# Kernel optimization log

Measured on AMD Instinct MI355X. Metric: run time of the kernel, lower is better.

The kernel has to match this reference:

```python
import jax, jax.numpy as jnp
import numpy as np

N_QUBITS = 14
N_LAYERS = 4
BATCH = 2048
DIM = 2 ** N_QUBITS


def setup_inputs() -> dict:
    key = jax.random.key(0)
    k1, k2 = jax.random.split(key)
    x = jax.random.normal(k1, (BATCH, N_QUBITS), dtype=jnp.float32)
    params = 2.0 * jnp.pi * jax.random.uniform(k2, (N_LAYERS, 1, N_QUBITS), dtype=jnp.float32)
    return {"x": x, "params": params}


def _angle_embed_x(x):
    """RX(x_q) angle embedding from |0...0>: product state, qubit 0 most significant."""
    B, n = x.shape
    c = jnp.cos(x / 2)
    s = jnp.sin(x / 2)
    state = jnp.ones((B, 1), dtype=jnp.complex64)
    for q in range(n):  # fixed small loop over qubits (kron build-up)
        amp = jnp.stack([c[:, q] + 0j, (-1j) * s[:, q]], axis=-1).astype(jnp.complex64)  # (B,2)
        state = (state[:, :, None] * amp[:, None, :]).reshape(B, -1)
    return state  # (B, 2^n)


def _apply_rx(state, theta, q, n):
    """Apply RX(theta) on qubit q to batched state (B, 2^n)."""
    c = jnp.cos(theta / 2).astype(jnp.complex64)
    s = ((-1j) * jnp.sin(theta / 2)).astype(jnp.complex64)
    B = state.shape[0]
    st = state.reshape(B, 2 ** q, 2, 2 ** (n - q - 1))
    a0, a1 = st[:, :, 0, :], st[:, :, 1, :]
    new = jnp.stack([c * a0 + s * a1, s * a0 + c * a1], axis=2)
    return new.reshape(B, -1)


def _apply_cnot(state, ctrl, tgt, n):
    B = state.shape[0]
    lo, hi = min(ctrl, tgt), max(ctrl, tgt)
    st = state.reshape(B, 2 ** lo, 2, 2 ** (hi - lo - 1), 2, 2 ** (n - hi - 1))
    if ctrl < tgt:
        # control axis=2, target axis=4: flip target where control==1
        flipped = st[:, :, 1, :, ::-1, :]
        st = jnp.stack([st[:, :, 0], flipped], axis=2)
    else:
        # control axis=4, target axis=2
        flipped = st[:, :, ::-1, :, 1, :]
        st = jnp.stack([st[:, :, :, :, 0, :], flipped], axis=4)
    return st.reshape(B, -1)


def _z_signs(n):
    # sign[q, k] = +1 if bit q (MSB-first) of k is 0 else -1
    k = np.arange(2 ** n)
    bits = (k[None, :] >> np.arange(n - 1, -1, -1)[:, None]) & 1
    return jnp.asarray(1.0 - 2.0 * bits, dtype=jnp.float32)  # (n, 2^n)


def reference(x, params):
    n = N_QUBITS
    state = _angle_embed_x(x)  # (B, 2^n) complex64
    for layer in range(N_LAYERS):
        w = params[layer, 0]  # (n,)
        for q in range(n):
            state = _apply_rx(state, w[q], q, n)
        for q in range(n):  # ring of CNOTs (basic entangling layer)
            state = _apply_cnot(state, q, (q + 1) % n, n)
    probs = state.real ** 2 + state.imag ** 2  # (B, 2^n)
    return probs @ _z_signs(n).T  # (B, n) per-qubit <Z>
```

## Files before the change

### kernel.cpp

```cpp
#include <hip/hip_runtime.h>
#include <hip/hip_fp16.h>
#include <stdint.h>

#define NQ     14
#define NL     4
#define BATCH  2048
#define DIM    16384

using half8  = __attribute__((ext_vector_type(8)))  _Float16;
using half4  = __attribute__((ext_vector_type(4)))  _Float16;
using f32x16 = __attribute__((ext_vector_type(16))) float;
using f32x4  = __attribute__((ext_vector_type(4)))  float;

constexpr uint32_t mmask(int b) { return b < 13 ? (((1u << (b + 1)) - 1u) | 0x2000u) : 0x1FFFu; }
constexpr uint32_t laddr(uint32_t a) {
  uint32_t col = a >> 5;
  uint32_t g = (a >> 2) & 7u;
  const uint32_t mx[9] = {1u, 2u, 4u, 2u, 0u, 0u, 1u, 2u, 4u};
  for (int j = 0; j < 9; ++j) if ((col >> j) & 1u) g ^= mx[j];
  return (col << 7) ^ (g << 4) ^ ((a & 3u) << 2);
}
constexpr uint32_t IMG(int b) { return laddr(mmask(b)); }

struct TabEmb { uint32_t v[32]; constexpr TabEmb() : v() {
  for (int k = 0; k < 32; ++k) { uint32_t x = 0;
    for (int b = 0; b < 5; ++b) if ((k >> b) & 1) x ^= IMG(b); v[k] = x; } } };
constexpr TabEmb EMBT{};

struct TabSc { uint32_t v[8][4]; constexpr TabSc() : v() {
  for (int i = 0; i < 8; ++i) for (int r = 0; r < 4; ++r) { uint32_t x = 0;
    if (r & 1) x ^= IMG(0); if (r & 2) x ^= IMG(1);
    if (i & 1) x ^= IMG(4); if (i & 2) x ^= IMG(5); if (i & 4) x ^= IMG(6);
    v[i][r] = x; } } };
constexpr TabSc SCT{};

struct TabEc { uint32_t v[16]; constexpr TabEc() : v() {
  for (int e = 0; e < 16; ++e) { uint32_t ce = (uint32_t)((e & 3) | ((e >> 2) << 3));
    v[e] = (ce << 6) ^ (((ce ^ (ce >> 2)) & 3u) << 4); } } };
constexpr TabEc ECT{};

__device__ __forceinline__ half8 h8(uint32_t a, uint32_t b, uint32_t c, uint32_t d) {
  union { uint32_t u[4]; half8 h; } z; z.u[0]=a; z.u[1]=b; z.u[2]=c; z.u[3]=d; return z.h; }
__device__ __forceinline__ half4 h4v(uint32_t a, uint32_t b) {
  union { uint32_t u[2]; half4 h; } z; z.u[0]=a; z.u[1]=b; return z.h; }
__device__ __forceinline__ uint4 ld16(const char* p) {
  return *(const uint4*)__builtin_assume_aligned(p, 16); }
__device__ __forceinline__ void st16(char* p, uint4 v) {
  *(uint4*)__builtin_assume_aligned(p, 16) = v; }
__device__ __forceinline__ uint32_t pkh2(float a, float b) {
  return __builtin_bit_cast(uint32_t, __floats2half2_rn(a, b)); }

__global__ void uprep_kernel(const float* __restrict__ params, __half* __restrict__ U) {
  const int id = blockIdx.x * 256 + threadIdx.x;
  int li, grp, r, k, nb, off, mstride;
  if (id < 6144) { li = id >> 11; const int sub = id & 2047;
    grp = sub >> 10; const int cell = sub & 1023; r = cell >> 5; k = cell & 31; nb = 5;
    off = li * 4608 + grp * 2048 + r * 32 + k; mstride = 1024; }
  else { const int id2 = id - 6144; li = id2 >> 8; const int cell = id2 & 255;
    grp = 2; r = cell >> 4; k = cell & 15; nb = 4;
    off = li * 4608 + 4096 + r * 16 + k; mstride = 256; }
  const float* th = params + (li + 1) * NQ;
  float mag = 1.f; int d = 0;
  for (int j = 0; j < nb; ++j) {
    const int pbit = (grp == 0) ? j : (grp == 1) ? 5 + j : 10 + j;
    const float ph = 0.5f * th[13 - pbit];
    const int df = ((r >> j) ^ (k >> j)) & 1;
    mag *= df ? sinf(ph) : cosf(ph);
    d += df;
  }
  float R = 0.f, I = 0.f;
  switch (d & 3) { case 0: R = mag; break; case 1: I = -mag; break;
                   case 2: R = -mag; break; default: I = mag; break; }
  U[off] = __float2half_rn(R);
  U[off + mstride] = __float2half_rn(I);
}

__global__ __launch_bounds__(512)
__attribute__((amdgpu_waves_per_eu(4, 4)))
void qsim_kernel(const float* __restrict__ x, const float* __restrict__ params,
                 const __half* __restrict__ U, float* __restrict__ out) {
  __shared__ uint32_t lds[DIM];
  __shared__ float red[8][16];
  __shared__ float exc[NQ], exs[NQ];
  char* const sb = (char*)lds;

  const int b = blockIdx.x;
  const int t = threadIdx.x;
  const int w = t >> 6, l = t & 63;
  const int hi = l >> 5, l31 = l & 31, l15 = l & 15, h4 = (l >> 4) & 3;
  const int swz = (l & 7) ^ ((l >> 2) & 2) ^ w;

  if (t < NQ) { const float xv = x[b * NQ + t] + params[t];
                exc[t] = cosf(0.5f * xv); exs[t] = sinf(0.5f * xv); }
  __syncthreads();

  const uint32_t colAB = (uint32_t)(((w << 6) | l31) << 7);
  const uint32_t sgl = (uint32_t)(((l15 ^ (l15 >> 2)) ^ w) & 3);
  const uint32_t gcr = (uint32_t)((w << 13) | (l15 << 6) | (((h4 ^ (int)sgl) & 3) << 4));
  const uint32_t lbc = ((uint32_t)l31 << 11) ^ ((uint32_t)hi << 8)
      ^ ((uint32_t)(((w >> 1) ^ ((l31 >> 2) & 3) ^ hi) & 3) << 4)
      ^ ((uint32_t)(((w << 1) ^ l) & 3) << 2);
  uint32_t scb = 0;
  { if (l & 16) scb ^= IMG(2);
    if (l & 32) scb ^= IMG(3);
#pragma unroll
    for (int j = 0; j < 4; ++j) if ((l15 >> j) & 1) scb ^= IMG(10 + j);
#pragma unroll
    for (int j = 0; j < 3; ++j) if ((w >> j) & 1) scb ^= IMG(7 + j); }

  const bool gcs0 = (l & 1), gcs1 = (l & 2);
  const uint32_t scb2 = scb ^ (gcs0 ? IMG(0) : 0u) ^ (gcs1 ? IMG(1) : 0u);
  const bool gbs0 = (l & 16), gbs1 = (l & 4);
  const uint32_t lbc2 = lbc ^ (gbs0 ? 0x50u : 0u) ^ (gbs1 ? 0xA0u : 0u);

  {
    float pb = 1.f;
#pragma unroll
    for (int j = 0; j < 9; ++j) pb *= ((t >> j) & 1) ? exs[8 - j] : exc[8 - j];
    uint32_t eb = 0;
#pragma unroll
    for (int j = 0; j < 9; ++j) if ((t >> j) & 1) eb ^= IMG(5 + j);
    const int tt = t & 31;
    const int sgk = ((tt & 1) ? 16 : 0) | ((tt & 2) ? 4 : 0) | ((tt & 4) ? 8 : 0)
                  | ((tt & 8) ? 2 : 0) | ((tt & 16) ? 1 : 0);
    if (sgk & 1)  eb ^= IMG(0);
    if (sgk & 2)  eb ^= IMG(1);
    if (sgk & 4)  eb ^= IMG(2);
    if (sgk & 8)  eb ^= IMG(3);
    if (sgk & 16) eb ^= IMG(4);
    const int pct = __popc(t);
#pragma unroll
    for (int k = 0; k < 32; ++k) {
      const int idx = k ^ sgk;
      float f = pb;
      f *= (idx & 1)  ? exs[13] : exc[13];
      f *= (idx & 2)  ? exs[12] : exc[12];
      f *= (idx & 4)  ? exs[11] : exc[11];
      f *= (idx & 8)  ? exs[10] : exc[10];
      f *= (idx & 16) ? exs[9]  : exc[9];
      const int pc = (pct + __popc(idx)) & 3;
      const float xr = (pc == 0) ? f : ((pc == 2) ? -f : 0.f);
      const float yi = (pc == 1) ? -f : ((pc == 3) ? f : 0.f);
      *(uint32_t*)(sb + (eb ^ EMBT.v[k])) = pkh2(xr, yi);
    }
  }
  __syncthreads();

#pragma unroll 1
  for (int li = 0; li < 3; ++li) {
    const __half* Ul = U + li * 4608;

    {
      half8 bR[2], bI[2];
#pragma unroll
      for (int s = 0; s < 2; ++s) {
        const __half* up = Ul + l31 * 32 + s * 16 + hi * 8;
        bR[s] = *(const half8*)__builtin_assume_aligned(up, 16);
        bI[s] = *(const half8*)__builtin_assume_aligned(up + 1024, 16);
      }
#pragma unroll
      for (int n = 0; n < 2; ++n) {
        const uint32_t cb = colAB + (uint32_t)(n << 12);
        f32x16 cX = {}, cY = {};
#pragma unroll
        for (int s = 0; s < 2; ++s) {
          const uint4 q0 = ld16(sb + cb + (uint32_t)((((s << 2) + (hi << 1) + 0) ^ swz) << 4));
          const uint4 q1 = ld16(sb + cb + (uint32_t)((((s << 2) + (hi << 1) + 1) ^ swz) << 4));
          const uint32_t dw[8] = {q0.x, q0.y, q0.z, q0.w, q1.x, q1.y, q1.z, q1.w};
          uint32_t ax[4], ay[4], an[4];
#pragma unroll
          for (int j = 0; j < 4; ++j) {
            ax[j] = __builtin_amdgcn_perm(dw[2 * j + 1], dw[2 * j], 0x05040100u);
            ay[j] = __builtin_amdgcn_perm(dw[2 * j + 1], dw[2 * j], 0x07060302u);
            an[j] = ay[j] ^ 0x80008000u;
          }
          const half8 aX = h8(ax[0], ax[1], ax[2], ax[3]);
          const half8 aY = h8(ay[0], ay[1], ay[2], ay[3]);
          const half8 aN = h8(an[0], an[1], an[2], an[3]);
          cX = __builtin_amdgcn_mfma_f32_32x32x16_f16(aX, bR[s], cX, 0, 0, 0);
          cX = __builtin_amdgcn_mfma_f32_32x32x16_f16(aN, bI[s], cX, 0, 0, 0);
          cY = __builtin_amdgcn_mfma_f32_32x32x16_f16(aX, bI[s], cY, 0, 0, 0);
          cY = __builtin_amdgcn_mfma_f32_32x32x16_f16(aY, bR[s], cY, 0, 0, 0);
        }
#pragma unroll
        for (int u = 0; u < 4; ++u) {
          uint4 o;
          o.x = pkh2(cX[4 * u + 0], cY[4 * u + 0]); o.y = pkh2(cX[4 * u + 1], cY[4 * u + 1]);
          o.z = pkh2(cX[4 * u + 2], cY[4 * u + 2]); o.w = pkh2(cX[4 * u + 3], cY[4 * u + 3]);
          st16(sb + cb + (uint32_t)((((u << 1) + hi) ^ swz) << 4), o);
        }
      }
      __builtin_amdgcn_wave_barrier();
    }

    {
      half8 bR[2], bI[2];
#pragma unroll
      for (int s = 0; s < 2; ++s) {
        const __half* up = Ul + 2048 + l31 * 32 + s * 16 + hi * 8;
        bR[s] = *(const half8*)__builtin_assume_aligned(up, 16);
        bI[s] = *(const half8*)__builtin_assume_aligned(up + 1024, 16);
      }
      uint4 dr[2][2][2];
#pragma unroll
      for (int n = 0; n < 2; ++n)
#pragma unroll
        for (int s = 0; s < 2; ++s)
#pragma unroll
          for (int j = 0; j < 2; ++j)
            dr[n][s][j] = ld16(sb + colAB + (uint32_t)(n << 12)
                               + (uint32_t)((((s << 2) + (hi << 1) + j) ^ swz) << 4));
      __syncthreads();
#pragma unroll
      for (int n = 0; n < 2; ++n) {
        f32x16 cX = {}, cY = {};
#pragma unroll
        for (int s = 0; s < 2; ++s) {
          const uint32_t dw[8] = {dr[n][s][0].x, dr[n][s][0].y, dr[n][s][0].z, dr[n][s][0].w,
                                  dr[n][s][1].x, dr[n][s][1].y, dr[n][s][1].z, dr[n][s][1].w};
          uint32_t ax[4], ay[4], an[4];
#pragma unroll
          for (int j = 0; j < 4; ++j) {
            ax[j] = __builtin_amdgcn_perm(dw[2 * j + 1], dw[2 * j], 0x05040100u);
            ay[j] = __builtin_amdgcn_perm(dw[2 * j + 1], dw[2 * j], 0x07060302u);
            an[j] = ay[j] ^ 0x80008000u;
          }
          const half8 aX = h8(ax[0], ax[1], ax[2], ax[3]);
          const half8 aY = h8(ay[0], ay[1], ay[2], ay[3]);
          const half8 aN = h8(an[0], an[1], an[2], an[3]);
          cX = __builtin_amdgcn_mfma_f32_32x32x16_f16(aX, bR[s], cX, 0, 0, 0);
          cX = __builtin_amdgcn_mfma_f32_32x32x16_f16(aN, bI[s], cX, 0, 0, 0);
          cY = __builtin_amdgcn_mfma_f32_32x32x16_f16(aX, bI[s], cY, 0, 0, 0);
          cY = __builtin_amdgcn_mfma_f32_32x32x16_f16(aY, bR[s], cY, 0, 0, 0);
        }
        const uint32_t lb = lbc2 ^ (uint32_t)(n << 2);
        uint32_t pk[16];
#pragma unroll
        for (int e = 0; e < 16; ++e) pk[e] = pkh2(cX[e], cY[e]);
#pragma unroll
        for (int q = 0; q < 4; ++q) {
          const uint32_t a0 = pk[4 * q + 0], a1 = pk[4 * q + 1];
          const uint32_t a2 = pk[4 * q + 2], a3 = pk[4 * q + 3];
          const uint32_t b0 = gbs0 ? a1 : a0, b1 = gbs0 ? a0 : a1;
          const uint32_t b2 = gbs0 ? a3 : a2, b3 = gbs0 ? a2 : a3;
          const uint32_t c0 = gbs1 ? b2 : b0, c1 = gbs1 ? b3 : b1;
          const uint32_t c2 = gbs1 ? b0 : b2, c3 = gbs1 ? b1 : b3;
          *(uint32_t*)(sb + (lb ^ ECT.v[4 * q + 0])) = c0;
          *(uint32_t*)(sb + (lb ^ ECT.v[4 * q + 1])) = c1;
          *(uint32_t*)(sb + (lb ^ ECT.v[4 * q + 2])) = c2;
          *(uint32_t*)(sb + (lb ^ ECT.v[4 * q + 3])) = c3;
        }
      }
      __syncthreads();
    }

    {
      const __half* up = Ul + 4096 + l15 * 16 + h4 * 4;
      const half4 bR = *(const half4*)__builtin_assume_aligned(up, 8);
      const half4 bI = *(const half4*)__builtin_assume_aligned(up + 256, 8);
      uint4 dc[8];
#pragma unroll
      for (int i = 0; i < 8; ++i)
        dc[i] = ld16(sb + gcr + (uint32_t)(i << 10));
      __syncthreads();
      float sE0[8], sE1[8], sE2[8];
#pragma unroll
      for (int i = 0; i < 8; ++i) {
        const int m2 = (i >> 1) & 3;
        const uint32_t ph[4] = {dc[i].x, dc[i].y, dc[i].z, dc[i].w};
        const uint32_t d0 = ph[0 ^ m2], d1 = ph[1 ^ m2], d2 = ph[2 ^ m2], d3 = ph[3 ^ m2];
        const uint32_t x0 = __builtin_amdgcn_perm(d1, d0, 0x05040100u);
        const uint32_t x1 = __builtin_amdgcn_perm(d3, d2, 0x05040100u);
        const uint32_t y0 = __builtin_amdgcn_perm(d1, d0, 0x07060302u);
        const uint32_t y1 = __builtin_amdgcn_perm(d3, d2, 0x07060302u);
        const half4 aX = h4v(x0, x1);
        const half4 aY = h4v(y0, y1);
        const half4 aN = h4v(y0 ^ 0x80008000u, y1 ^ 0x80008000u);
        f32x4 cX = {}, cY = {};
        cX = __builtin_amdgcn_mfma_f32_16x16x16f16(aX, bR, cX, 0, 0, 0);
        cX = __builtin_amdgcn_mfma_f32_16x16x16f16(aN, bI, cX, 0, 0, 0);
        cY = __builtin_amdgcn_mfma_f32_16x16x16f16(aX, bI, cY, 0, 0, 0);
        cY = __builtin_amdgcn_mfma_f32_16x16x16f16(aY, bR, cY, 0, 0, 0);
        if (li < 2) {
          const uint32_t p0 = pkh2(cX[0], cY[0]), p1 = pkh2(cX[1], cY[1]);
          const uint32_t p2 = pkh2(cX[2], cY[2]), p3 = pkh2(cX[3], cY[3]);
          const uint32_t q0 = gcs0 ? p1 : p0, q1 = gcs0 ? p0 : p1;
          const uint32_t q2 = gcs0 ? p3 : p2, q3 = gcs0 ? p2 : p3;
          const uint32_t r0 = gcs1 ? q2 : q0, r1 = gcs1 ? q3 : q1;
          const uint32_t r2 = gcs1 ? q0 : q2, r3 = gcs1 ? q1 : q3;
          *(uint32_t*)(sb + (scb2 ^ SCT.v[i][0])) = r0;
          *(uint32_t*)(sb + (scb2 ^ SCT.v[i][1])) = r1;
          *(uint32_t*)(sb + (scb2 ^ SCT.v[i][2])) = r2;
          *(uint32_t*)(sb + (scb2 ^ SCT.v[i][3])) = r3;
        } else {
          const float p0 = fmaf(cX[0], cX[0], cY[0] * cY[0]);
          const float p1 = fmaf(cX[1], cX[1], cY[1] * cY[1]);
          const float p2 = fmaf(cX[2], cX[2], cY[2] * cY[2]);
          const float p3 = fmaf(cX[3], cX[3], cY[3] * cY[3]);
          const float t01 = p0 + p1, t23 = p2 + p3;
          const float d01 = p0 - p1, d23 = p2 - p3;
          sE0[i] = t01 + t23;
          sE1[i] = t01 - t23;
          sE2[i] = d01 - d23;
        }
      }
      if (li < 2) {
        __syncthreads();
      } else {
        float A = 0.f, Bv = 0.f, Cv = 0.f;
#pragma unroll
        for (int i = 0; i < 8; ++i) {
          if (__popc(i) & 1) { A -= sE2[i]; Bv -= sE1[i]; Cv -= sE0[i]; }
          else               { A += sE2[i]; Bv += sE1[i]; Cv += sE0[i]; }
        }
        const float u0 = sE0[0] + sE0[1], u1 = sE0[2] + sE0[3];
        const float u2 = sE0[4] + sE0[5], u3 = sE0[6] + sE0[7];
        float Dv = (u0 - u1) - (u2 - u3);
        float Ev = (u0 + u1) - (u2 + u3);
        float Fv = (u0 + u1) + (u2 + u3);
#pragma unroll
        for (int m = 0; m < 6; ++m) {
          const int hb = 1 << m;
          const bool up2 = (l & hb) != 0;
          float u;
          u = __shfl_xor(A, hb, 64);  A  = up2 ? (u - A)  : (u + A);
          u = __shfl_xor(Bv, hb, 64); Bv = up2 ? (u - Bv) : (u + Bv);
          u = __shfl_xor(Cv, hb, 64); Cv = up2 ? (u - Cv) : (u + Cv);
          u = __shfl_xor(Dv, hb, 64); Dv = up2 ? (u - Dv) : (u + Dv);
          u = __shfl_xor(Ev, hb, 64); Ev = up2 ? (u - Ev) : (u + Ev);
          u = __shfl_xor(Fv, hb, 64); Fv = up2 ? (u - Fv) : (u + Fv);
        }
        const float swv = (__popc(w) & 1) ? -1.f : 1.f;
        if (l == 63)      { red[w][13] = swv * A; red[w][12] = swv * Bv; red[w][11] = swv * Cv; }
        else if (l == 55) { red[w][0]  = swv * A; }
        else if (l == 47) { red[w][10] = swv * Cv; }
        else if (l == 15) { red[w][9] = swv * Cv; red[w][8] = swv * Dv; red[w][7] = swv * Ev;
                            red[w][6] = swv * Fv;
                            red[w][5] = (__popc(w >> 1) & 1) ? -Fv : Fv;
                            red[w][4] = ((w >> 2) & 1) ? -Fv : Fv;
                            red[w][3] = Fv; }
        else if (l == 14) { red[w][2] = Fv; }
        else if (l == 12) { red[w][1] = Fv; }
      }
    }
  }

  __syncthreads();
  if (t < NQ) {
    float sq = 0.f;
#pragma unroll
    for (int ww = 0; ww < 8; ++ww) sq += red[ww][t];
    out[b * NQ + t] = sq;
  }
}

extern "C" void kernel_launch(void* const* d_in, const int* in_sizes, int n_in,
                              void* d_out, int out_size, void* d_ws, size_t ws_size,
                              hipStream_t stream) {
  const float* x      = (const float*)d_in[0];
  const float* params = (const float*)d_in[1];
  float* out          = (float*)d_out;
  __half* U           = (__half*)d_ws;
  uprep_kernel<<<27, 256, 0, stream>>>(params, U);
  qsim_kernel<<<BATCH, 512, 0, stream>>>(x, params, (const __half*)U, out);
}
```

Baseline: 154.1 us.

## Fuse first two MFMA gate stages via register lane swaps instead of LDS round-trip

The first and second 5-qubit unitary stages are fused so the first stage's MFMA output is passed straight to the second through permlane32_swap (or a shfl_xor fallback), with no LDS store and reload in between. This removes one LDS write/read pass and a wave barrier per layer. B-fragments for both stages are loaded up front, which raises register pressure and may lower occupancy.

```diff
diff --git a/kernel.cpp b/kernel.cpp
--- a/kernel.cpp
+++ b/kernel.cpp
@@ -11,6 +11,7 @@
 using half4  = __attribute__((ext_vector_type(4)))  _Float16;
 using f32x16 = __attribute__((ext_vector_type(16))) float;
 using f32x4  = __attribute__((ext_vector_type(4)))  float;
+using u32v2  = __attribute__((ext_vector_type(2)))  unsigned int;
 
 constexpr uint32_t mmask(int b) { return b < 13 ? (((1u << (b + 1)) - 1u) | 0x2000u) : 0x1FFFu; }
 constexpr uint32_t laddr(uint32_t a) {
@@ -49,6 +50,20 @@
   *(uint4*)__builtin_assume_aligned(p, 16) = v; }
 __device__ __forceinline__ uint32_t pkh2(float a, float b) {
   return __builtin_bit_cast(uint32_t, __floats2half2_rn(a, b)); }
+
+__device__ __forceinline__ void hswap(uint32_t a, uint32_t b, uint32_t& r0, uint32_t& r1,
+                                      int hi) {
+#if __has_builtin(__builtin_amdgcn_permlane32_swap)
+  u32v2 rr = __builtin_amdgcn_permlane32_swap(a, b, false, false);
+  r0 = rr[0]; r1 = rr[1];
+  (void)hi;
+#else
+  const uint32_t send = hi ? b : a;
+  const uint32_t recv = (uint32_t)__shfl_xor((int)send, 32, 64);
+  r0 = hi ? recv : a;
+  r1 = hi ? b : recv;
+#endif
+}
 
 __global__ void uprep_kernel(const float* __restrict__ params, __half* __restrict__ U) {
   const int id = blockIdx.x * 256 + threadIdx.x;
@@ -150,109 +165,96 @@
   for (int li = 0; li < 3; ++li) {
     const __half* Ul = U + li * 4608;
 
-    {
-      half8 bR[2], bI[2];
+    half8 aRf[2], aIf[2], bRf[2], bIf[2];
+#pragma unroll
+    for (int s = 0; s < 2; ++s) {
+      const __half* upA = Ul + l31 * 32 + s * 16 + hi * 8;
+      aRf[s] = *(const half8*)__builtin_assume_aligned(upA, 16);
+      aIf[s] = *(const half8*)__builtin_assume_aligned(upA + 1024, 16);
+      const __half* upB = Ul + 2048 + l31 * 32 + s * 16 + hi * 8;
+      bRf[s] = *(const half8*)__builtin_assume_aligned(upB, 16);
+      bIf[s] = *(const half8*)__builtin_assume_aligned(upB + 1024, 16);
+    }
+
+    uint4 ga[2][2][2];
+#pragma unroll
+    for (int n = 0; n < 2; ++n)
+#pragma unroll
+      for (int s = 0; s < 2; ++s)
+#pragma unroll
+        for (int j = 0; j < 2; ++j)
+          ga[n][s][j] = ld16(sb + colAB + (uint32_t)(n << 12)
+                             + (uint32_t)((((s << 2) + (hi << 1) + j) ^ swz) << 4));
+    __syncthreads();
+
+#pragma unroll
+    for (int n = 0; n < 2; ++n) {
+      f32x16 cX = {}, cY = {};
 #pragma unroll
       for (int s = 0; s < 2; ++s) {
-        const __half* up = Ul + l31 * 32 + s * 16 + hi * 8;
-        bR[s] = *(const half8*)__builtin_assume_aligned(up, 16);
-        bI[s] = *(const half8*)__builtin_assume_aligned(up + 1024, 16);
-      }
-#pragma unroll
-      for (int n = 0; n < 2; ++n) {
-        const uint32_t cb = colAB + (uint32_t)(n << 12);
-        f32x16 cX = {}, cY = {};
-#pragma unroll
-        for (int s = 0; s < 2; ++s) {
-          const uint4 q0 = ld16(sb + cb + (uint32_t)((((s << 2) + (hi << 1) + 0) ^ swz) << 4));
-          const uint4 q1 = ld16(sb + cb + (uint32_t)((((s << 2) + (hi << 1) + 1) ^ swz) << 4));
-          const uint32_t dw[8] = {q0.x, q0.y, q0.z, q0.w, q1.x, q1.y, q1.z, q1.w};
-          uint32_t ax[4], ay[4], an[4];
-#pragma unroll
-          for (int j = 0; j < 4; ++j) {
-            ax[j] = __builtin_amdgcn_perm(dw[2 * j + 1], dw[2 * j], 0x05040100u);
-            ay[j] = __builtin_amdgcn_perm(dw[2 * j + 1], dw[2 * j], 0x07060302u);
-            an[j] = ay[j] ^ 0x80008000u;
-          }
-          const half8 aX = h8(ax[0], ax[1], ax[2], ax[3]);
-          const half8 aY = h8(ay[0], ay[1], ay[2], ay[3]);
-          const half8 aN = h8(an[0], an[1], an[2], an[3]);
-          cX = __builtin_amdgcn_mfma_f32_32x32x16_f16(aX, bR[s], cX, 0, 0, 0);
-          cX = __builtin_amdgcn_mfma_f32_32x32x16_f16(aN, bI[s], cX, 0, 0, 0);
-          cY = __builtin_amdgcn_mfma_f32_32x32x16_f16(aX, bI[s], cY, 0, 0, 0);
-          cY = __builtin_amdgcn_mfma_f32_32x32x16_f16(aY, bR[s], cY, 0, 0, 0);
-        }
-#pragma unroll
-        for (int u = 0; u < 4; ++u) {
-          uint4 o;
-          o.x = pkh2(cX[4 * u + 0], cY[4 * u + 0]); o.y = pkh2(cX[4 * u + 1], cY[4 * u + 1]);
-          o.z = pkh2(cX[4 * u + 2], cY[4 * u + 2]); o.w = pkh2(cX[4 * u + 3], cY[4 * u + 3]);
-          st16(sb + cb + (uint32_t)((((u << 1) + hi) ^ swz) << 4), o);
-        }
-      }
-      __builtin_amdgcn_wave_barrier();
+        const uint32_t dwg[8] = {ga[n][s][0].x, ga[n][s][0].y, ga[n][s][0].z, ga[n][s][0].w,
+                                 ga[n][s][1].x, ga[n][s][1].y, ga[n][s][1].z, ga[n][s][1].w};
+        uint32_t ax[4], ay[4], an[4];
+#pragma unroll
+        for (int j = 0; j < 4; ++j) {
+          ax[j] = __builtin_amdgcn_perm(dwg[2 * j + 1], dwg[2 * j], 0x05040100u);
+          ay[j] = __builtin_amdgcn_perm(dwg[2 * j + 1], dwg[2 * j], 0x07060302u);
+          an[j] = ay[j] ^ 0x80008000u;
+        }
+        const half8 aX = h8(ax[0], ax[1], ax[2], ax[3]);
+        const half8 aY = h8(ay[0], ay[1], ay[2], ay[3]);
+        const half8 aN = h8(an[0], an[1], an[2], an[3]);
+        cX = __builtin_amdgcn_mfma_f32_32x32x16_f16(aX, aRf[s], cX, 0, 0, 0);
+        cX = __builtin_amdgcn_mfma_f32_32x32x16_f16(aN, aIf[s], cX, 0, 0, 0);
+        cY = __builtin_amdgcn_mfma_f32_32x32x16_f16(aX, aIf[s], cY, 0, 0, 0);
+        cY = __builtin_amdgcn_mfma_f32_32x32x16_f16(aY, aRf[s], cY, 0, 0, 0);
+      }
+      uint32_t pk[16];
+#pragma unroll
+      for (int e = 0; e < 16; ++e) pk[e] = pkh2(cX[e], cY[e]);
+
+      f32x16 dX = {}, dY = {};
+#pragma unroll
+      for (int s = 0; s < 2; ++s) {
+        uint32_t dw[8];
+#pragma unroll
+        for (int j = 0; j < 4; ++j)
+          hswap(pk[8 * s + j], pk[8 * s + 4 + j], dw[j], dw[4 + j], hi);
+        uint32_t ax[4], ay[4], an[4];
+#pragma unroll
+        for (int j = 0; j < 4; ++j) {
+          ax[j] = __builtin_amdgcn_perm(dw[2 * j + 1], dw[2 * j], 0x05040100u);
+          ay[j] = __builtin_amdgcn_perm(dw[2 * j + 1], dw[2 * j], 0x07060302u);
+          an[j] = ay[j] ^ 0x80008000u;
+        }
+        const half8 aX = h8(ax[0], ax[1], ax[2], ax[3]);
+        const half8 aY = h8(ay[0], ay[1], ay[2], ay[3]);
+        const half8 aN = h8(an[0], an[1], an[2], an[3]);
+        dX = __builtin_amdgcn_mfma_f32_32x32x16_f16(aX, bRf[s], dX, 0, 0, 0);
+        dX = __builtin_amdgcn_mfma_f32_32x32x16_f16(aN, bIf[s], dX, 0, 0, 0);
+        dY = __builtin_amdgcn_mfma_f32_32x32x16_f16(aX, bIf[s], dY, 0, 0, 0);
+        dY = __builtin_amdgcn_mfma_f32_32x32x16_f16(aY, bRf[s], dY, 0, 0, 0);
+      }
+
+      const uint32_t lb = lbc2 ^ (uint32_t)(n << 2);
+      uint32_t pk2[16];
+#pragma unroll
+      for (int e = 0; e < 16; ++e) pk2[e] = pkh2(dX[e], dY[e]);
+#pragma unroll
+      for (int q = 0; q < 4; ++q) {
+        const uint32_t a0 = pk2[4 * q + 0], a1 = pk2[4 * q + 1];
+        const uint32_t a2 = pk2[4 * q + 2], a3 = pk2[4 * q + 3];
+        const uint32_t b0 = gbs0 ? a1 : a0, b1 = gbs0 ? a0 : a1;
+        const uint32_t b2 = gbs0 ? a3 : a2, b3 = gbs0 ? a2 : a3;
+        const uint32_t c0 = gbs1 ? b2 : b0, c1 = gbs1 ? b3 : b1;
+        const uint32_t c2 = gbs1 ? b0 : b2, c3 = gbs1 ? b1 : b3;
+        *(uint32_t*)(sb + (lb ^ ECT.v[4 * q + 0])) = c0;
+        *(uint32_t*)(sb + (lb ^ ECT.v[4 * q + 1])) = c1;
+        *(uint32_t*)(sb + (lb ^ ECT.v[4 * q + 2])) = c2;
+        *(uint32_t*)(sb + (lb ^ ECT.v[4 * q + 3])) = c3;
+      }
     }
-
-    {
-      half8 bR[2], bI[2];
-#pragma unroll
-      for (int s = 0; s < 2; ++s) {
-        const __half* up = Ul + 2048 + l31 * 32 + s * 16 + hi * 8;
-        bR[s] = *(const half8*)__builtin_assume_aligned(up, 16);
-        bI[s] = *(const half8*)__builtin_assume_aligned(up + 1024, 16);
-      }
-      uint4 dr[2][2][2];
-#pragma unroll
-      for (int n = 0; n < 2; ++n)
-#pragma unroll
-        for (int s = 0; s < 2; ++s)
-#pragma unroll
-          for (int j = 0; j < 2; ++j)
-            dr[n][s][j] = ld16(sb + colAB + (uint32_t)(n << 12)
-                               + (uint32_t)((((s << 2) + (hi << 1) + j) ^ swz) << 4));
-      __syncthreads();
-#pragma unroll
-      for (int n = 0; n < 2; ++n) {
-        f32x16 cX = {}, cY = {};
-#pragma unroll
-        for (int s = 0; s < 2; ++s) {
-          const uint32_t dw[8] = {dr[n][s][0].x, dr[n][s][0].y, dr[n][s][0].z, dr[n][s][0].w,
-                                  dr[n][s][1].x, dr[n][s][1].y, dr[n][s][1].z, dr[n][s][1].w};
-          uint32_t ax[4], ay[4], an[4];
-#pragma unroll
-          for (int j = 0; j < 4; ++j) {
-            ax[j] = __builtin_amdgcn_perm(dw[2 * j + 1], dw[2 * j], 0x05040100u);
-            ay[j] = __builtin_amdgcn_perm(dw[2 * j + 1], dw[2 * j], 0x07060302u);
-            an[j] = ay[j] ^ 0x80008000u;
-          }
-          const half8 aX = h8(ax[0], ax[1], ax[2], ax[3]);
-          const half8 aY = h8(ay[0], ay[1], ay[2], ay[3]);
-          const half8 aN = h8(an[0], an[1], an[2], an[3]);
-          cX = __builtin_amdgcn_mfma_f32_32x32x16_f16(aX, bR[s], cX, 0, 0, 0);
-          cX = __builtin_amdgcn_mfma_f32_32x32x16_f16(aN, bI[s], cX, 0, 0, 0);
-          cY = __builtin_amdgcn_mfma_f32_32x32x16_f16(aX, bI[s], cY, 0, 0, 0);
-          cY = __builtin_amdgcn_mfma_f32_32x32x16_f16(aY, bR[s], cY, 0, 0, 0);
-        }
-        const uint32_t lb = lbc2 ^ (uint32_t)(n << 2);
-        uint32_t pk[16];
-#pragma unroll
-        for (int e = 0; e < 16; ++e) pk[e] = pkh2(cX[e], cY[e]);
-#pragma unroll
-        for (int q = 0; q < 4; ++q) {
-          const uint32_t a0 = pk[4 * q + 0], a1 = pk[4 * q + 1];
-          const uint32_t a2 = pk[4 * q + 2], a3 = pk[4 * q + 3];
-          const uint32_t b0 = gbs0 ? a1 : a0, b1 = gbs0 ? a0 : a1;
-          const uint32_t b2 = gbs0 ? a3 : a2, b3 = gbs0 ? a2 : a3;
-          const uint32_t c0 = gbs1 ? b2 : b0, c1 = gbs1 ? b3 : b1;
-          const uint32_t c2 = gbs1 ? b0 : b2, c3 = gbs1 ? b1 : b3;
-          *(uint32_t*)(sb + (lb ^ ECT.v[4 * q + 0])) = c0;
-          *(uint32_t*)(sb + (lb ^ ECT.v[4 * q + 1])) = c1;
-          *(uint32_t*)(sb + (lb ^ ECT.v[4 * q + 2])) = c2;
-          *(uint32_t*)(sb + (lb ^ ECT.v[4 * q + 3])) = c3;
-        }
-      }
-      __syncthreads();
-    }
+    __syncthreads();
 
     {
       const __half* up = Ul + 4096 + l15 * 16 + h4 * 4;
```

Result: slower. 159.6 us (+3.6%).
